# Optimization experiments

Hardware: AMD Instinct MI355X
Metric: run time of the kernel (lower is better)

The kernel has to match this reference:

```python
import jax, jax.numpy as jnp
import numpy as np

CONF_THRES = 0.45
IOU_THRES = 0.45
K = 1000      # candidate cap after confidence filtering (top-K by score)
MAX_DET = 300 # max detections kept per image


def setup_inputs() -> dict:
    key = jax.random.key(0)
    k1, k2 = jax.random.split(key)
    B, N, NC = 16, 25200, 80
    p = jax.random.uniform(k1, (B, N, 5 + NC), dtype=jnp.float32)
    # scale xywh to realistic pixel coords: cx,cy in [0,640), w,h in [0,128)
    scale = jnp.concatenate([jnp.array([640.0, 640.0, 128.0, 128.0], jnp.float32),
                             jnp.ones((1 + NC,), jnp.float32)])
    prediction = p * scale
    logits = jax.random.normal(k2, (B, N, NC), dtype=jnp.float32)
    return {"prediction": prediction, "logits": logits}


def xywh2xyxy(x):
    cx, cy, w, h = x[..., 0], x[..., 1], x[..., 2], x[..., 3]
    return jnp.stack([cx - w / 2, cy - h / 2, cx + w / 2, cy + h / 2], axis=-1)


def box_iou(a, b):
    # a: [K,4], b: [K,4] in xyxy -> [K,K]
    area_a = (a[:, 2] - a[:, 0]) * (a[:, 3] - a[:, 1])
    area_b = (b[:, 2] - b[:, 0]) * (b[:, 3] - b[:, 1])
    lt = jnp.maximum(a[:, None, :2], b[None, :, :2])
    rb = jnp.minimum(a[:, None, 2:], b[None, :, 2:])
    wh = jnp.clip(rb - lt, 0.0)
    inter = wh[..., 0] * wh[..., 1]
    return inter / (area_a[:, None] + area_b[None, :] - inter + 1e-9)


def _nms_image(pred, log):
    # pred: [N, 5+nc], log: [N, nc]
    obj = pred[:, 4]
    cls_scores = pred[:, 5:] * obj[:, None]          # x[:,5:] *= x[:,4:5]
    conf = jnp.max(cls_scores, axis=-1)
    j = jnp.argmax(cls_scores, axis=-1)
    box = xywh2xyxy(pred[:, :4])
    valid = (obj > CONF_THRES) & (conf > CONF_THRES)
    score = jnp.where(valid, conf, -1.0)
    sc, idx = jax.lax.top_k(score, K)                # descending, as torchvision nms sorts
    b = box[idx]                                     # [K,4]
    c = j[idx]                                       # [K]
    lg = log[idx]                                    # [K,nc]
    v = sc > 0.0
    iou = box_iou(b, b)                              # [K,K]
    ar = jnp.arange(K)

    def body(i, state):
        keep, supp = state
        alive = jnp.logical_not(supp[i])
        keep = keep.at[i].set(alive)
        supp = supp | (alive & (iou[i] > IOU_THRES) & (ar > i))
        return keep, supp

    keep, _ = jax.lax.fori_loop(0, K, body, (jnp.zeros((K,), bool), jnp.logical_not(v)))
    ksc = jnp.where(keep, sc, -1.0)
    fsc, fidx = jax.lax.top_k(ksc, MAX_DET)
    m = fsc > 0.0                                    # validity mask per detection row
    det = jnp.concatenate([b[fidx], sc[fidx][:, None], c[fidx].astype(jnp.float32)[:, None]], axis=1)
    det = jnp.where(m[:, None], det, 0.0)            # padded rows = zeros((0,6)) analogue
    lgo = jnp.where(m[:, None], lg[fidx], 0.0)
    return det, m, lgo


def reference(prediction, logits):
    # det: [B, MAX_DET, 6] (x1,y1,x2,y2,conf,cls), mask: [B, MAX_DET], logits_out: [B, MAX_DET, nc]
    det, mask, logits_out = jax.vmap(_nms_image)(prediction, logits)
    return det, mask, logits_out
```

## Files before the change

kernel.cpp:

```cpp
#include <hip/hip_runtime.h>
#include <hip/hip_bf16.h>

#define BATCH 16
#define NCAND 25200
#define NCLS 80
#define PREDC 85
#define KTOP 1000
#define MAXDET 300
#define CAP 2048
#define NBINS 1024
#define TILE_ROWS 128
#define CONF 0.45f
#define HSCALE ((float)NBINS / (1.0f - 0.45f))
#define CNT_STRIDE 16

typedef unsigned long long ull;

__global__ __launch_bounds__(256) void k_score(const float* __restrict__ pred,
                                               float* __restrict__ score,
                                               float* __restrict__ bx,
                                               int* __restrict__ cls) {
    __shared__ float lds[TILE_ROWS * PREDC];
    int tile = blockIdx.x;
    int tid = threadIdx.x;
    size_t base = (size_t)tile * (TILE_ROWS * PREDC);
    const float4* src4 = (const float4*)(pred + base);
    float4* l4 = (float4*)lds;
    const int NV4 = TILE_ROWS * PREDC / 4;
    for (int k = tid; k < NV4; k += 256) l4[k] = src4[k];
    __syncthreads();
    if (tid < TILE_ROWS) {
        const float* row = lds + tid * PREDC;
        float obj = row[4];
        float best = -1.0f; int bj = 0;
        #pragma unroll 8
        for (int c = 0; c < NCLS; ++c) {
            float v = row[5 + c] * obj;
            if (v > best) { best = v; bj = c; }
        }
        bool valid = (obj > CONF) && (best > CONF);
        float s = valid ? best : -1.0f;
        int grow = tile * TILE_ROWS + tid;
        score[grow] = s;
        cls[grow] = bj;
        float cx = row[0], cy = row[1], w = row[2], h = row[3];
        ((float4*)bx)[grow] = make_float4(cx - w * 0.5f, cy - h * 0.5f,
                                          cx + w * 0.5f, cy + h * 0.5f);
    }
}

__device__ __forceinline__ void cmpx(ull& r, ull p, bool keepMin) {
    ull mn = r < p ? r : p;
    ull mx = r < p ? p : r;
    r = keepMin ? mn : mx;
}

__global__ __launch_bounds__(1024) void k_topk(const float* __restrict__ score,
                                               const float* __restrict__ bx,
                                               const int* __restrict__ cls,
                                               int* __restrict__ topidx,
                                               float* __restrict__ topsc,
                                               int* __restrict__ topcls,
                                               float* __restrict__ boxes,
                                               int* __restrict__ cnt) {
    __shared__ int hist[NBINS];
    __shared__ ull sbuf[CAP];
    __shared__ int s_T, s_base;
    int b = blockIdx.x, tid = threadIdx.x;
    int lane = tid & 63;
    const float* sc = score + (size_t)b * NCAND;
    const float4* sc4 = (const float4*)sc;
    const int NF4 = NCAND / 4;
    hist[tid] = 0;
    if (tid == 0) { s_T = 0; s_base = 0; }
    __syncthreads();
    for (int f = tid; f < NF4; f += 1024) {
        float4 v4 = sc4[f];
        float vs[4] = {v4.x, v4.y, v4.z, v4.w};
        #pragma unroll
        for (int e = 0; e < 4; ++e) {
            float s = vs[e];
            if (s > CONF) {
                int bin = (int)((s - CONF) * HSCALE);
                bin = bin < 0 ? 0 : (bin > NBINS - 1 ? NBINS - 1 : bin);
                atomicAdd(&hist[bin], 1);
            }
        }
    }
    __syncthreads();
    for (int off = 1; off < NBINS; off <<= 1) {
        int v = (tid + off < NBINS) ? hist[tid + off] : 0;
        __syncthreads();
        hist[tid] += v;
        __syncthreads();
    }
    {
        int S = hist[tid];
        int Sn = (tid + 1 < NBINS) ? hist[tid + 1] : 0;
        if (S >= KTOP && Sn < KTOP) s_T = tid;
    }
    sbuf[tid] = ~0ULL;
    sbuf[tid + 1024] = ~0ULL;
    __syncthreads();
    int T = s_T;
    for (int f = tid; f < NF4; f += 1024) {
        float4 v4 = sc4[f];
        float vs[4] = {v4.x, v4.y, v4.z, v4.w};
        #pragma unroll
        for (int e = 0; e < 4; ++e) {
            float s = vs[e];
            bool want = false;
            if (s > CONF) {
                int bin = (int)((s - CONF) * HSCALE);
                bin = bin < 0 ? 0 : (bin > NBINS - 1 ? NBINS - 1 : bin);
                want = (bin >= T);
            }
            ull m = __ballot(want);
            int wb = 0;
            if (lane == 0 && m) wb = atomicAdd(&s_base, (int)__popcll(m));
            wb = __shfl(wb, 0);
            if (want) {
                int pos = wb + (int)__popcll(m & ((1ULL << lane) - 1ULL));
                if (pos < CAP) {
                    unsigned sb2 = __float_as_uint(s);
                    sbuf[pos] = ((ull)(~sb2) << 32) | (unsigned)(f * 4 + e);
                }
            }
        }
    }
    __syncthreads();
    int C2 = s_base; if (C2 > CAP) C2 = CAP;
    ull r0 = sbuf[tid];
    ull r1 = sbuf[tid + 1024];
    int t2 = tid + 1024;
    #pragma unroll
    for (unsigned k = 2; k <= 64; k <<= 1) {
        #pragma unroll
        for (unsigned j = k >> 1; j > 0; j >>= 1) {
            ull p0 = __shfl_xor(r0, (int)j);
            ull p1 = __shfl_xor(r1, (int)j);
            bool amLow = ((tid & j) == 0);
            cmpx(r0, p0, amLow == ((tid & k) == 0));
            cmpx(r1, p1, amLow == ((t2 & k) == 0));
        }
    }
    #pragma unroll
    for (unsigned k = 128; k <= 1024; k <<= 1) {
        #pragma unroll
        for (unsigned j = k >> 1; j >= 64; j >>= 1) {
            sbuf[tid] = r0; sbuf[t2] = r1;
            __syncthreads();
            ull p0 = sbuf[tid ^ j];
            ull p1 = sbuf[t2 ^ j];
            cmpx(r0, p0, ((tid & j) == 0) == ((tid & k) == 0));
            cmpx(r1, p1, ((t2 & j) == 0) == ((t2 & k) == 0));
            __syncthreads();
        }
        #pragma unroll
        for (unsigned j = 32; j > 0; j >>= 1) {
            ull p0 = __shfl_xor(r0, (int)j);
            ull p1 = __shfl_xor(r1, (int)j);
            bool amLow = ((tid & j) == 0);
            cmpx(r0, p0, amLow == ((tid & k) == 0));
            cmpx(r1, p1, amLow == ((t2 & k) == 0));
        }
    }
    {
        if (r1 < r0) { ull t = r0; r0 = r1; r1 = t; }
        #pragma unroll
        for (unsigned j = 512; j >= 64; j >>= 1) {
            sbuf[tid] = r0; sbuf[t2] = r1;
            __syncthreads();
            ull p0 = sbuf[tid ^ j];
            ull p1 = sbuf[t2 ^ j];
            cmpx(r0, p0, ((tid & j) == 0));
            cmpx(r1, p1, ((t2 & j) == 0));
            __syncthreads();
        }
        #pragma unroll
        for (unsigned j = 32; j > 0; j >>= 1) {
            ull p0 = __shfl_xor(r0, (int)j);
            ull p1 = __shfl_xor(r1, (int)j);
            bool amLow = ((tid & j) == 0);
            cmpx(r0, p0, amLow);
            cmpx(r1, p1, amLow);
        }
    }
    if (tid < KTOP) {
        int o = b * KTOP + tid;
        if (tid < C2) {
            int n = (int)(r0 & 0xFFFFFFFFULL);
            float s = __uint_as_float(~(unsigned)(r0 >> 32));
            topidx[o] = n;
            topsc[o] = s;
            topcls[o] = cls[b * NCAND + n];
            ((float4*)boxes)[o] = ((const float4*)bx)[b * NCAND + n];
        } else {
            topidx[o] = 0; topsc[o] = -1.0f; topcls[o] = 0;
            ((float4*)boxes)[o] = make_float4(0.f, 0.f, 0.f, 0.f);
        }
    }
    if (tid == 0) cnt[b * CNT_STRIDE] = C2;
}

__global__ __launch_bounds__(256) void k_iou(const float* __restrict__ boxes,
                                             ull* __restrict__ M) {
    #pragma clang fp contract(off)
    int g = blockIdx.x * 256 + threadIdx.x;
    int w = g & 15;
    int bi = g >> 4;
    int i = bi % KTOP;
    int b = bi / KTOP;
    int j0 = w * 64;
    if (j0 + 63 <= i) {
        M[(size_t)bi * 16 + w] = 0ULL;
        return;
    }
    const float4* bxp = (const float4*)boxes + (size_t)b * KTOP;
    float4 A = bxp[i];
    float areaA = (A.z - A.x) * (A.w - A.y);
    ull word = 0;
    int jend = j0 + 64; if (jend > KTOP) jend = KTOP;
    #pragma unroll 4
    for (int j = j0; j < jend; ++j) {
        float4 Bb = bxp[j];
        float areaB = (Bb.z - Bb.x) * (Bb.w - Bb.y);
        float lx = fmaxf(A.x, Bb.x), ly = fmaxf(A.y, Bb.y);
        float rx = fminf(A.z, Bb.z), ry = fminf(A.w, Bb.w);
        float ww = rx - lx; ww = ww > 0.f ? ww : 0.f;
        float hh = ry - ly; hh = hh > 0.f ? hh : 0.f;
        float inter = ww * hh;
        float denom = ((areaA + areaB) - inter) + 1e-9f;
        float iou = inter / denom;
        if (j > i && iou > 0.45f) word |= 1ULL << (j - j0);
    }
    M[(size_t)bi * 16 + w] = word;
}

__global__ __launch_bounds__(1024) void k_nms_out(const ull* __restrict__ M,
                                                  const int* __restrict__ cnt,
                                                  const float* __restrict__ logits,
                                                  const int* __restrict__ topidx,
                                                  const float* __restrict__ topsc,
                                                  const int* __restrict__ topcls,
                                                  const float* __restrict__ boxes,
                                                  float* __restrict__ out) {
    __shared__ ull buf[2][64 * 17];
    __shared__ ull s_keep[16];
    __shared__ int kept_r[MAXDET];
    __shared__ int kept_n[MAXDET];
    __shared__ int s_kc;
    int b = blockIdx.x, tid = threadIdx.x;
    int kc0 = cnt[b * CNT_STRIDE]; if (kc0 > KTOP) kc0 = KTOP;
    const ull* Mb = M + (size_t)b * KTOP * 16;
    buf[0][(tid >> 4) * 17 + (tid & 15)] = Mb[tid];
    __syncthreads();
    ull supp;
    {
        int w = tid & 15, lo = w * 64;
        if (kc0 <= lo) supp = ~0ULL;
        else if (kc0 >= lo + 64) supp = 0ULL;
        else supp = (~0ULL) << (kc0 - lo);
    }
    for (int rb = 0; rb < 16; ++rb) {
        int cur = rb & 1, nxt = cur ^ 1;
        if (tid >= 64) {
            if (rb < 15) {
                for (int u = tid - 64; u < 1024; u += 960) {
                    int idx = (rb + 1) * 1024 + u;
                    int g = idx < 16000 ? idx : 15999;
                    buf[nxt][(u >> 4) * 17 + (u & 15)] = Mb[g];
                }
            }
        } else {
            int l = tid, w = l & 15, q = l >> 4;
            const ull* B = buf[cur];
            ull drow = B[l * 17 + rb];
            ull crow[16];
            #pragma unroll
            for (int k = 0; k < 16; ++k) crow[k] = B[(q + 4 * k) * 17 + w];
            int slo = (int)(supp & 0xffffffffULL);
            int shi = (int)(supp >> 32);
            unsigned rlo = (unsigned)__builtin_amdgcn_readlane(slo, rb)
                         | (unsigned)__builtin_amdgcn_readlane(slo, rb + 16)
                         | (unsigned)__builtin_amdgcn_readlane(slo, rb + 32)
                         | (unsigned)__builtin_amdgcn_readlane(slo, rb + 48);
            unsigned rhi = (unsigned)__builtin_amdgcn_readlane(shi, rb)
                         | (unsigned)__builtin_amdgcn_readlane(shi, rb + 16)
                         | (unsigned)__builtin_amdgcn_readlane(shi, rb + 32)
                         | (unsigned)__builtin_amdgcn_readlane(shi, rb + 48);
            ull removed = ((ull)rhi << 32) | rlo;
            int dlo_v = (int)(drow & 0xffffffffULL);
            int dhi_v = (int)(drow >> 32);
            #pragma unroll
            for (int s = 0; s < 64; ++s) {
                unsigned dl = (unsigned)__builtin_amdgcn_readlane(dlo_v, s);
                unsigned dh = (unsigned)__builtin_amdgcn_readlane(dhi_v, s);
                ull d64 = ((ull)dh << 32) | dl;
                if (!((removed >> s) & 1ULL)) removed |= d64;
            }
            ull acc = 0;
            #pragma unroll
            for (int k = 0; k < 16; ++k) {
                int r = q + 4 * k;
                if (!((removed >> r) & 1ULL)) acc |= crow[k];
            }
            supp |= acc;
        }
        __syncthreads();
    }
    if (tid < 64) {
        supp |= __shfl_xor(supp, 16);
        supp |= __shfl_xor(supp, 32);
        if (tid < 16) s_keep[tid] = ~supp;
    }
    __syncthreads();
    if (tid < 16) {
        int pre = 0;
        for (int u = 0; u < tid; ++u) pre += __popcll(s_keep[u]);
        ull wv = s_keep[tid];
        int rank = pre;
        while (wv) {
            int bit = __builtin_ctzll(wv);
            if (rank < MAXDET) kept_r[rank] = tid * 64 + bit;
            rank++;
            wv &= wv - 1;
        }
        if (tid == 15) s_kc = rank < MAXDET ? rank : MAXDET;
    }
    __syncthreads();
    int kc = s_kc;
    if (tid < MAXDET && tid < kc) kept_n[tid] = topidx[b * KTOP + kept_r[tid]];
    __syncthreads();
    float* det = out;
    float* mask_o = out + BATCH * MAXDET * 6;
    float* lgo = out + BATCH * MAXDET * 6 + BATCH * MAXDET;
    for (int idx = tid; idx < MAXDET * 6; idx += 1024) {
        int s = idx / 6, col = idx % 6;
        float v = 0.f;
        if (s < kc) {
            int o = b * KTOP + kept_r[s];
            if (col < 4) v = boxes[o * 4 + col];
            else if (col == 4) v = topsc[o];
            else v = (float)topcls[o];
        }
        det[b * MAXDET * 6 + idx] = v;
    }
    for (int s = tid; s < MAXDET; s += 1024)
        mask_o[b * MAXDET + s] = (s < kc) ? 1.0f : 0.0f;
    float4* lgo4 = (float4*)(lgo + (size_t)b * MAXDET * NCLS);
    const float4* lg4 = (const float4*)logits;
    for (int idx = tid; idx < MAXDET * (NCLS / 4); idx += 1024) {
        int s = idx / (NCLS / 4), cc = idx % (NCLS / 4);
        float4 v = make_float4(0.f, 0.f, 0.f, 0.f);
        if (s < kc) v = lg4[((size_t)b * NCAND + kept_n[s]) * (NCLS / 4) + cc];
        lgo4[idx] = v;
    }
}

extern "C" void kernel_launch(void* const* d_in, const int* in_sizes, int n_in,
                              void* d_out, int out_size, void* d_ws, size_t ws_size,
                              hipStream_t stream) {
    (void)in_sizes; (void)n_in; (void)out_size; (void)ws_size;
    const float* pred = (const float*)d_in[0];
    const float* logits = (const float*)d_in[1];
    float* out = (float*)d_out;
    char* ws = (char*)d_ws;

    float* score  = (float*)(ws + 0);
    float* bx     = (float*)(ws + 1612800);
    int*   cls    = (int*)(ws + 8064000);
    ull*   M      = (ull*)(ws + 0);
    int*   cnt    = (int*)(ws + 9676800);
    int*   topidx = (int*)(ws + 9677824);
    float* topsc  = (float*)(ws + 9741824);
    int*   topcls = (int*)(ws + 9805824);
    float* boxes  = (float*)(ws + 9869824);

    const int nrows = BATCH * NCAND;
    k_score<<<nrows / TILE_ROWS, 256, 0, stream>>>(pred, score, bx, cls);
    k_topk<<<BATCH, 1024, 0, stream>>>(score, bx, cls, topidx, topsc, topcls, boxes, cnt);
    k_iou<<<(BATCH * KTOP * 16) / 256, 256, 0, stream>>>(boxes, M);
    k_nms_out<<<BATCH, 1024, 0, stream>>>(M, cnt, logits, topidx, topsc, topcls, boxes, out);
}
```

Baseline: 131.2 us.

## Fuse histogram into scoring and compute IoU bitmask on the fly in NMS

The score kernel now uses two threads per row, each reducing half the classes with a shuffle merge, and builds the per-image score histogram with global atomics. This removes the histogram pass from the single-block-per-image top-k kernel. The separate IoU kernel and its global bitmask are dropped: the NMS kernel loads the 1000 boxes into shared memory and computes each 64-bit suppression word while it double-buffers the previous row block. The trade-offs are an added memset launch, contention on global atomics, and IoU work moved onto only 16 blocks instead of a wide grid.

New measurement: 426.9 us. +225.3%, slower.

```diff
diff --git a/kernel.cpp b/kernel.cpp
--- a/kernel.cpp
+++ b/kernel.cpp
@@ -9,43 +9,59 @@
 #define MAXDET 300
 #define CAP 2048
 #define NBINS 1024
-#define TILE_ROWS 128
+#define SROWS 64
 #define CONF 0.45f
 #define HSCALE ((float)NBINS / (1.0f - 0.45f))
 #define CNT_STRIDE 16
 
 typedef unsigned long long ull;
 
-__global__ __launch_bounds__(256) void k_score(const float* __restrict__ pred,
+__global__ __launch_bounds__(128) void k_score(const float* __restrict__ pred,
                                                float* __restrict__ score,
                                                float* __restrict__ bx,
-                                               int* __restrict__ cls) {
-    __shared__ float lds[TILE_ROWS * PREDC];
+                                               int* __restrict__ cls,
+                                               int* __restrict__ hist) {
+    __shared__ float lds[SROWS * PREDC];
     int tile = blockIdx.x;
     int tid = threadIdx.x;
-    size_t base = (size_t)tile * (TILE_ROWS * PREDC);
+    size_t base = (size_t)tile * (SROWS * PREDC);
     const float4* src4 = (const float4*)(pred + base);
     float4* l4 = (float4*)lds;
-    const int NV4 = TILE_ROWS * PREDC / 4;
-    for (int k = tid; k < NV4; k += 256) l4[k] = src4[k];
-    __syncthreads();
-    if (tid < TILE_ROWS) {
-        const float* row = lds + tid * PREDC;
-        float obj = row[4];
-        float best = -1.0f; int bj = 0;
-        #pragma unroll 8
-        for (int c = 0; c < NCLS; ++c) {
-            float v = row[5 + c] * obj;
-            if (v > best) { best = v; bj = c; }
-        }
+    const int NV4 = SROWS * PREDC / 4;
+    for (int k = tid; k < NV4; k += 128) l4[k] = src4[k];
+    __syncthreads();
+    int r = tid >> 1, h = tid & 1;
+    const float* row = lds + r * PREDC;
+    float obj = row[4];
+    float best = -1.0f; int bj = 0;
+    int c0 = h * 40;
+    #pragma unroll 8
+    for (int c = 0; c < 40; ++c) {
+        float v = row[5 + c0 + c] * obj;
+        if (v > best) { best = v; bj = c0 + c; }
+    }
+    float obest = __shfl_xor(best, 1);
+    int obj2 = __shfl_xor(bj, 1);
+    if (h == 0) {
+        if (obest > best) { best = obest; bj = obj2; }
+    } else {
+        if (best > obest) {  } else { best = obest; bj = obj2; }
+    }
+    if (h == 0) {
         bool valid = (obj > CONF) && (best > CONF);
         float s = valid ? best : -1.0f;
-        int grow = tile * TILE_ROWS + tid;
+        int grow = tile * SROWS + r;
         score[grow] = s;
         cls[grow] = bj;
-        float cx = row[0], cy = row[1], w = row[2], h = row[3];
-        ((float4*)bx)[grow] = make_float4(cx - w * 0.5f, cy - h * 0.5f,
-                                          cx + w * 0.5f, cy + h * 0.5f);
+        float cx = row[0], cy = row[1], w = row[2], hh = row[3];
+        ((float4*)bx)[grow] = make_float4(cx - w * 0.5f, cy - hh * 0.5f,
+                                          cx + w * 0.5f, cy + hh * 0.5f);
+        if (s > CONF) {
+            int b = grow / NCAND;
+            int bin = (int)((s - CONF) * HSCALE);
+            bin = bin < 0 ? 0 : (bin > NBINS - 1 ? NBINS - 1 : bin);
+            atomicAdd(&hist[b * NBINS + bin], 1);
+        }
     }
 }
 
@@ -58,6 +74,7 @@
 __global__ __launch_bounds__(1024) void k_topk(const float* __restrict__ score,
                                                const float* __restrict__ bx,
                                                const int* __restrict__ cls,
+                                               const int* __restrict__ hist_g,
                                                int* __restrict__ topidx,
                                                float* __restrict__ topsc,
                                                int* __restrict__ topcls,
@@ -71,22 +88,8 @@
     const float* sc = score + (size_t)b * NCAND;
     const float4* sc4 = (const float4*)sc;
     const int NF4 = NCAND / 4;
-    hist[tid] = 0;
+    hist[tid] = hist_g[b * NBINS + tid];
     if (tid == 0) { s_T = 0; s_base = 0; }
-    __syncthreads();
-    for (int f = tid; f < NF4; f += 1024) {
-        float4 v4 = sc4[f];
-        float vs[4] = {v4.x, v4.y, v4.z, v4.w};
-        #pragma unroll
-        for (int e = 0; e < 4; ++e) {
-            float s = vs[e];
-            if (s > CONF) {
-                int bin = (int)((s - CONF) * HSCALE);
-                bin = bin < 0 ? 0 : (bin > NBINS - 1 ? NBINS - 1 : bin);
-                atomicAdd(&hist[bin], 1);
-            }
-        }
-    }
     __syncthreads();
     for (int off = 1; off < NBINS; off <<= 1) {
         int v = (tid + off < NBINS) ? hist[tid + off] : 0;
@@ -203,27 +206,16 @@
     if (tid == 0) cnt[b * CNT_STRIDE] = C2;
 }
 
-__global__ __launch_bounds__(256) void k_iou(const float* __restrict__ boxes,
-                                             ull* __restrict__ M) {
+__device__ __forceinline__ ull iou_word(const float4* __restrict__ bxl, int r, int w) {
     #pragma clang fp contract(off)
-    int g = blockIdx.x * 256 + threadIdx.x;
-    int w = g & 15;
-    int bi = g >> 4;
-    int i = bi % KTOP;
-    int b = bi / KTOP;
     int j0 = w * 64;
-    if (j0 + 63 <= i) {
-        M[(size_t)bi * 16 + w] = 0ULL;
-        return;
-    }
-    const float4* bxp = (const float4*)boxes + (size_t)b * KTOP;
-    float4 A = bxp[i];
+    if (j0 + 63 <= r) return 0ULL;
+    float4 A = bxl[r];
     float areaA = (A.z - A.x) * (A.w - A.y);
     ull word = 0;
-    int jend = j0 + 64; if (jend > KTOP) jend = KTOP;
     #pragma unroll 4
-    for (int j = j0; j < jend; ++j) {
-        float4 Bb = bxp[j];
+    for (int j = j0; j < j0 + 64; ++j) {
+        float4 Bb = bxl[j];
         float areaB = (Bb.z - Bb.x) * (Bb.w - Bb.y);
         float lx = fmaxf(A.x, Bb.x), ly = fmaxf(A.y, Bb.y);
         float rx = fminf(A.z, Bb.z), ry = fminf(A.w, Bb.w);
@@ -232,19 +224,19 @@
         float inter = ww * hh;
         float denom = ((areaA + areaB) - inter) + 1e-9f;
         float iou = inter / denom;
-        if (j > i && iou > 0.45f) word |= 1ULL << (j - j0);
-    }
-    M[(size_t)bi * 16 + w] = word;
-}
-
-__global__ __launch_bounds__(1024) void k_nms_out(const ull* __restrict__ M,
-                                                  const int* __restrict__ cnt,
+        if (j > r && iou > 0.45f) word |= 1ULL << (j - j0);
+    }
+    return word;
+}
+
+__global__ __launch_bounds__(1024) void k_nms_out(const int* __restrict__ cnt,
                                                   const float* __restrict__ logits,
                                                   const int* __restrict__ topidx,
                                                   const float* __restrict__ topsc,
                                                   const int* __restrict__ topcls,
                                                   const float* __restrict__ boxes,
                                                   float* __restrict__ out) {
+    __shared__ float4 bxl[1024];
     __shared__ ull buf[2][64 * 17];
     __shared__ ull s_keep[16];
     __shared__ int kept_r[MAXDET];
@@ -252,8 +244,10 @@
     __shared__ int s_kc;
     int b = blockIdx.x, tid = threadIdx.x;
     int kc0 = cnt[b * CNT_STRIDE]; if (kc0 > KTOP) kc0 = KTOP;
-    const ull* Mb = M + (size_t)b * KTOP * 16;
-    buf[0][(tid >> 4) * 17 + (tid & 15)] = Mb[tid];
+    bxl[tid] = (tid < KTOP) ? ((const float4*)boxes)[b * KTOP + tid]
+                            : make_float4(0.f, 0.f, 0.f, 0.f);
+    __syncthreads();
+    buf[0][(tid >> 4) * 17 + (tid & 15)] = iou_word(bxl, tid >> 4, tid & 15);
     __syncthreads();
     ull supp;
     {
@@ -266,11 +260,9 @@
         int cur = rb & 1, nxt = cur ^ 1;
         if (tid >= 64) {
             if (rb < 15) {
-                for (int u = tid - 64; u < 1024; u += 960) {
-                    int idx = (rb + 1) * 1024 + u;
-                    int g = idx < 16000 ? idx : 15999;
-                    buf[nxt][(u >> 4) * 17 + (u & 15)] = Mb[g];
-                }
+                for (int u = tid - 64; u < 1024; u += 960)
+                    buf[nxt][(u >> 4) * 17 + (u & 15)] =
+                        iou_word(bxl, (rb + 1) * 64 + (u >> 4), u & 15);
             }
         } else {
             int l = tid, w = l & 15, q = l >> 4;
@@ -370,16 +362,16 @@
     float* score  = (float*)(ws + 0);
     float* bx     = (float*)(ws + 1612800);
     int*   cls    = (int*)(ws + 8064000);
-    ull*   M      = (ull*)(ws + 0);
-    int*   cnt    = (int*)(ws + 9676800);
-    int*   topidx = (int*)(ws + 9677824);
-    float* topsc  = (float*)(ws + 9741824);
-    int*   topcls = (int*)(ws + 9805824);
-    float* boxes  = (float*)(ws + 9869824);
+    int*   hist   = (int*)(ws + 9676800);
+    int*   cnt    = (int*)(ws + 9742336);
+    int*   topidx = (int*)(ws + 9743360);
+    float* topsc  = (float*)(ws + 9807360);
+    int*   topcls = (int*)(ws + 9871360);
+    float* boxes  = (float*)(ws + 9935360);
 
     const int nrows = BATCH * NCAND;
-    k_score<<<nrows / TILE_ROWS, 256, 0, stream>>>(pred, score, bx, cls);
-    k_topk<<<BATCH, 1024, 0, stream>>>(score, bx, cls, topidx, topsc, topcls, boxes, cnt);
-    k_iou<<<(BATCH * KTOP * 16) / 256, 256, 0, stream>>>(boxes, M);
-    k_nms_out<<<BATCH, 1024, 0, stream>>>(M, cnt, logits, topidx, topsc, topcls, boxes, out);
-}
+    hipMemsetAsync(hist, 0, BATCH * NBINS * sizeof(int), stream);
+    k_score<<<nrows / SROWS, 128, 0, stream>>>(pred, score, bx, cls, hist);
+    k_topk<<<BATCH, 1024, 0, stream>>>(score, bx, cls, hist, topidx, topsc, topcls, boxes, cnt);
+    k_nms_out<<<BATCH, 1024, 0, stream>>>(cnt, logits, topidx, topsc, topcls, boxes, out);
+}
```

## Add single-register sort path for small candidate counts and register-prefetch NMS matrix

Applied to the files above, without the earlier changes.

The top-K bitonic sort now takes a cheaper one-element-per-thread 1024-wide path when the filtered candidate count fits in 1024, keeping the two-element 2048 path only as a fallback. Separately, the NMS kernel's producer threads prefetch the next suppression-matrix block into registers one iteration ahead, so global loads overlap the consumer's work instead of being issued and stored in the same step. The costs are more code and register pressure, plus a branch on the candidate count.

New measurement: 124.0 us. 1.06x faster.

```diff
diff --git a/kernel.cpp b/kernel.cpp
--- a/kernel.cpp
+++ b/kernel.cpp
@@ -130,67 +130,113 @@
     }
     __syncthreads();
     int C2 = s_base; if (C2 > CAP) C2 = CAP;
-    ull r0 = sbuf[tid];
-    ull r1 = sbuf[tid + 1024];
-    int t2 = tid + 1024;
-    #pragma unroll
-    for (unsigned k = 2; k <= 64; k <<= 1) {
-        #pragma unroll
-        for (unsigned j = k >> 1; j > 0; j >>= 1) {
-            ull p0 = __shfl_xor(r0, (int)j);
-            ull p1 = __shfl_xor(r1, (int)j);
-            bool amLow = ((tid & j) == 0);
-            cmpx(r0, p0, amLow == ((tid & k) == 0));
-            cmpx(r1, p1, amLow == ((t2 & k) == 0));
-        }
-    }
-    #pragma unroll
-    for (unsigned k = 128; k <= 1024; k <<= 1) {
-        #pragma unroll
-        for (unsigned j = k >> 1; j >= 64; j >>= 1) {
-            sbuf[tid] = r0; sbuf[t2] = r1;
+    ull key0;
+    if (C2 <= 1024) {
+        ull r0 = sbuf[tid];
+        #pragma unroll
+        for (unsigned k = 2; k <= 64; k <<= 1) {
+            #pragma unroll
+            for (unsigned j = k >> 1; j > 0; j >>= 1) {
+                ull p0 = __shfl_xor(r0, (int)j);
+                bool amLow = ((tid & j) == 0);
+                cmpx(r0, p0, amLow == ((tid & k) == 0));
+            }
+        }
+        #pragma unroll
+        for (unsigned k = 128; k <= 512; k <<= 1) {
+            #pragma unroll
+            for (unsigned j = k >> 1; j >= 64; j >>= 1) {
+                sbuf[tid] = r0;
+                __syncthreads();
+                ull p0 = sbuf[tid ^ j];
+                cmpx(r0, p0, ((tid & j) == 0) == ((tid & k) == 0));
+                __syncthreads();
+            }
+            #pragma unroll
+            for (unsigned j = 32; j > 0; j >>= 1) {
+                ull p0 = __shfl_xor(r0, (int)j);
+                bool amLow = ((tid & j) == 0);
+                cmpx(r0, p0, amLow == ((tid & k) == 0));
+            }
+        }
+        #pragma unroll
+        for (unsigned j = 512; j >= 64; j >>= 1) {
+            sbuf[tid] = r0;
             __syncthreads();
             ull p0 = sbuf[tid ^ j];
-            ull p1 = sbuf[t2 ^ j];
-            cmpx(r0, p0, ((tid & j) == 0) == ((tid & k) == 0));
-            cmpx(r1, p1, ((t2 & j) == 0) == ((t2 & k) == 0));
+            cmpx(r0, p0, ((tid & j) == 0));
             __syncthreads();
         }
         #pragma unroll
         for (unsigned j = 32; j > 0; j >>= 1) {
             ull p0 = __shfl_xor(r0, (int)j);
-            ull p1 = __shfl_xor(r1, (int)j);
-            bool amLow = ((tid & j) == 0);
-            cmpx(r0, p0, amLow == ((tid & k) == 0));
-            cmpx(r1, p1, amLow == ((t2 & k) == 0));
-        }
-    }
-    {
-        if (r1 < r0) { ull t = r0; r0 = r1; r1 = t; }
-        #pragma unroll
-        for (unsigned j = 512; j >= 64; j >>= 1) {
-            sbuf[tid] = r0; sbuf[t2] = r1;
-            __syncthreads();
-            ull p0 = sbuf[tid ^ j];
-            ull p1 = sbuf[t2 ^ j];
             cmpx(r0, p0, ((tid & j) == 0));
-            cmpx(r1, p1, ((t2 & j) == 0));
-            __syncthreads();
-        }
-        #pragma unroll
-        for (unsigned j = 32; j > 0; j >>= 1) {
-            ull p0 = __shfl_xor(r0, (int)j);
-            ull p1 = __shfl_xor(r1, (int)j);
-            bool amLow = ((tid & j) == 0);
-            cmpx(r0, p0, amLow);
-            cmpx(r1, p1, amLow);
-        }
+        }
+        key0 = r0;
+    } else {
+        ull r0 = sbuf[tid];
+        ull r1 = sbuf[tid + 1024];
+        int t2 = tid + 1024;
+        #pragma unroll
+        for (unsigned k = 2; k <= 64; k <<= 1) {
+            #pragma unroll
+            for (unsigned j = k >> 1; j > 0; j >>= 1) {
+                ull p0 = __shfl_xor(r0, (int)j);
+                ull p1 = __shfl_xor(r1, (int)j);
+                bool amLow = ((tid & j) == 0);
+                cmpx(r0, p0, amLow == ((tid & k) == 0));
+                cmpx(r1, p1, amLow == ((t2 & k) == 0));
+            }
+        }
+        #pragma unroll
+        for (unsigned k = 128; k <= 1024; k <<= 1) {
+            #pragma unroll
+            for (unsigned j = k >> 1; j >= 64; j >>= 1) {
+                sbuf[tid] = r0; sbuf[t2] = r1;
+                __syncthreads();
+                ull p0 = sbuf[tid ^ j];
+                ull p1 = sbuf[t2 ^ j];
+                cmpx(r0, p0, ((tid & j) == 0) == ((tid & k) == 0));
+                cmpx(r1, p1, ((t2 & j) == 0) == ((t2 & k) == 0));
+                __syncthreads();
+            }
+            #pragma unroll
+            for (unsigned j = 32; j > 0; j >>= 1) {
+                ull p0 = __shfl_xor(r0, (int)j);
+                ull p1 = __shfl_xor(r1, (int)j);
+                bool amLow = ((tid & j) == 0);
+                cmpx(r0, p0, amLow == ((tid & k) == 0));
+                cmpx(r1, p1, amLow == ((t2 & k) == 0));
+            }
+        }
+        {
+            if (r1 < r0) { ull t = r0; r0 = r1; r1 = t; }
+            #pragma unroll
+            for (unsigned j = 512; j >= 64; j >>= 1) {
+                sbuf[tid] = r0; sbuf[t2] = r1;
+                __syncthreads();
+                ull p0 = sbuf[tid ^ j];
+                ull p1 = sbuf[t2 ^ j];
+                cmpx(r0, p0, ((tid & j) == 0));
+                cmpx(r1, p1, ((t2 & j) == 0));
+                __syncthreads();
+            }
+            #pragma unroll
+            for (unsigned j = 32; j > 0; j >>= 1) {
+                ull p0 = __shfl_xor(r0, (int)j);
+                ull p1 = __shfl_xor(r1, (int)j);
+                bool amLow = ((tid & j) == 0);
+                cmpx(r0, p0, amLow);
+                cmpx(r1, p1, amLow);
+            }
+        }
+        key0 = r0;
     }
     if (tid < KTOP) {
         int o = b * KTOP + tid;
         if (tid < C2) {
-            int n = (int)(r0 & 0xFFFFFFFFULL);
-            float s = __uint_as_float(~(unsigned)(r0 >> 32));
+            int n = (int)(key0 & 0xFFFFFFFFULL);
+            float s = __uint_as_float(~(unsigned)(key0 >> 32));
             topidx[o] = n;
             topsc[o] = s;
             topcls[o] = cls[b * NCAND + n];
@@ -254,6 +300,16 @@
     int kc0 = cnt[b * CNT_STRIDE]; if (kc0 > KTOP) kc0 = KTOP;
     const ull* Mb = M + (size_t)b * KTOP * 16;
     buf[0][(tid >> 4) * 17 + (tid & 15)] = Mb[tid];
+    int st = tid - 64;
+    ull v0 = 0, v1 = 0;
+    if (tid >= 64) {
+        int g0 = 1024 + st;
+        v0 = Mb[g0 < 16000 ? g0 : 15999];
+        if (st < 64) {
+            int g1 = 1024 + 960 + st;
+            v1 = Mb[g1 < 16000 ? g1 : 15999];
+        }
+    }
     __syncthreads();
     ull supp;
     {
@@ -266,10 +322,18 @@
         int cur = rb & 1, nxt = cur ^ 1;
         if (tid >= 64) {
             if (rb < 15) {
-                for (int u = tid - 64; u < 1024; u += 960) {
-                    int idx = (rb + 1) * 1024 + u;
-                    int g = idx < 16000 ? idx : 15999;
-                    buf[nxt][(u >> 4) * 17 + (u & 15)] = Mb[g];
+                buf[nxt][(st >> 4) * 17 + (st & 15)] = v0;
+                if (st < 64) {
+                    int u1 = 960 + st;
+                    buf[nxt][(u1 >> 4) * 17 + (u1 & 15)] = v1;
+                }
+                if (rb + 2 < 16) {
+                    int g0 = (rb + 2) * 1024 + st;
+                    v0 = Mb[g0 < 16000 ? g0 : 15999];
+                    if (st < 64) {
+                        int g1 = (rb + 2) * 1024 + 960 + st;
+                        v1 = Mb[g1 < 16000 ? g1 : 15999];
+                    }
                 }
             }
         } else {
```
